# Kernel optimization log

Hardware: AMD Instinct MI355X
Metric: run time of the kernel (lower is better)

## Reference

```python
import jax, jax.numpy as jnp
import numpy as np

B, S, D, H = 2, 2048, 1024, 16
HD = D // H  # head dim = 64


def setup_inputs() -> dict:
    key = jax.random.key(0)
    k0, k1, k2 = jax.random.split(key, 3)
    x = jax.random.normal(k0, (B, S, D), dtype=jnp.float32)
    # fused QKV projection: nn.Linear(D, 3D) -> weight [3D, D], bias [3D]
    Wqkv_w = jax.random.normal(k1, (3 * D, D), dtype=jnp.float32) * (1.0 / np.sqrt(D))
    Wqkv_b = jnp.zeros((3 * D,), dtype=jnp.float32)
    out_w = jax.random.normal(k2, (D, D), dtype=jnp.float32) * (1.0 / np.sqrt(D))
    out_b = jnp.zeros((D,), dtype=jnp.float32)
    # ALiBi-like additive bias, shape [1, H, 1, S] (broadcasts over queries)
    slopes = 2.0 ** (-8.0 * jnp.arange(1, H + 1, dtype=jnp.float32) / H)  # [H]
    dist = (S - 1) - jnp.arange(S, dtype=jnp.float32)                      # [S]
    attn_bias = (-slopes[:, None] * dist[None, :]).reshape(1, H, 1, S)
    # key padding mask: second sequence is padded by 256 tokens at the end
    lengths = jnp.array([S, S - 256])
    attention_mask = jnp.arange(S)[None, :] < lengths[:, None]             # [B, S] bool
    return {"x": x, "Wqkv_w": Wqkv_w, "Wqkv_b": Wqkv_b, "out_w": out_w,
            "out_b": out_b, "attn_bias": attn_bias, "attention_mask": attention_mask}


def reference(x, Wqkv_w, Wqkv_b, out_w, out_b, attn_bias, attention_mask):
    b, s, d = x.shape
    # fused QKV projection, then chunk into q, k, v along feature dim
    qkv = jnp.einsum('bsd,ed->bse', x, Wqkv_w) + Wqkv_b  # [b, s, 3d]
    q, k, v = jnp.split(qkv, 3, axis=-1)
    # b s (h hd) -> b h s hd
    q = q.reshape(b, s, H, HD).transpose(0, 2, 1, 3)
    k = k.reshape(b, s, H, HD).transpose(0, 2, 1, 3)
    v = v.reshape(b, s, H, HD).transpose(0, 2, 1, 3)
    softmax_scale = 1.0 / np.sqrt(HD)
    aw = jnp.einsum('bhqe,bhke->bhqk', q, k) * softmax_scale  # [b, H, s, s]
    aw = aw + attn_bias  # attn_bias broadcasts [1,H,1,s] -> [b,H,s,s]
    min_val = jnp.finfo(aw.dtype).min
    # key padding mask: mask positions where attention_mask is False
    aw = jnp.where(attention_mask[:, None, None, :], aw, min_val)
    # causal mask (is_causal=True, s_q == s_k)
    causal = jnp.tril(jnp.ones((s, s), dtype=bool))
    aw = jnp.where(causal[None, None, :, :], aw, min_val)
    p = jax.nn.softmax(aw, axis=-1)
    out = jnp.einsum('bhqk,bhke->bhqe', p, v)  # [b, H, s, HD]
    out = out.transpose(0, 2, 1, 3).reshape(b, s, d)
    return jnp.einsum('bsd,ed->bse', out, out_w) + out_b
```

## Files before the change

### kernel.cpp

```cpp
#include <hip/hip_runtime.h>
#include <hip/hip_bf16.h>
#include <stdint.h>

typedef __attribute__((ext_vector_type(8))) short s16x8;
typedef __attribute__((ext_vector_type(8))) unsigned short u16x8;
typedef __attribute__((ext_vector_type(4))) float f32x4;

#define SEQ 2048
#define LOG2E 1.44269504088896f

__device__ __forceinline__ unsigned short f2b(float x) {
  union { __hip_bfloat16 h; unsigned short u; } cv;
  cv.h = __float2bfloat16(x);
  return cv.u;
}

__device__ __forceinline__ float exp2fast(float x) {
  float r;
  asm("v_exp_f32 %0, %1" : "=v"(r) : "v"(x));
  return r;
}

__device__ __forceinline__ void gload16(const void* g, void* l) {
  __builtin_amdgcn_global_load_lds(
      (const __attribute__((address_space(1))) void*)g,
      (__attribute__((address_space(3))) void*)l, 16, 0, 0);
}

__global__ void cvt_all(const float* __restrict__ x, const float* __restrict__ wq,
                        const float* __restrict__ ow, const float* __restrict__ abias,
                        const void* __restrict__ maskp,
                        __hip_bfloat16* __restrict__ xb, __hip_bfloat16* __restrict__ wqb,
                        __hip_bfloat16* __restrict__ owb, float* __restrict__ biasm) {
  const int i = blockIdx.x * 256 + threadIdx.x;
  if (i >= 2097152) {
    const int j = i - 2097152;
    const int b = j >> 15, h = (j >> 11) & 15, kv = j & 2047;
    const int* mi = (const int*)maskp;
    const unsigned char* mb = (const unsigned char*)maskp;
    const bool int_fmt = (mi[0] == 0 || mi[0] == 1);
    const bool ok = int_fmt ? (mi[b * SEQ + kv] != 0) : (mb[b * SEQ + kv] != 0);
    biasm[j] = ok ? abias[h * SEQ + kv] * LOG2E : -1e30f;
    return;
  }
  const float* src;
  __hip_bfloat16* dst;
  int off;
  if (i < 1048576) { src = x; dst = xb; off = i; }
  else if (i < 1835008) { src = wq; dst = wqb; off = i - 1048576; }
  else { src = ow; dst = owb; off = i - 1835008; }
  float4 v = reinterpret_cast<const float4*>(src)[off];
  ushort4 o;
  o.x = f2b(v.x); o.y = f2b(v.y); o.z = f2b(v.z); o.w = f2b(v.w);
  reinterpret_cast<ushort4*>(dst)[off] = o;
}

template <int MODE, int BM>
__global__ __launch_bounds__(256) void gemm_bt(
    const __hip_bfloat16* __restrict__ A, const __hip_bfloat16* __restrict__ B,
    const float* __restrict__ bias, void* __restrict__ Cout,
    __hip_bfloat16* __restrict__ Vt, int M, int N, int K) {
  constexpr int MR = BM / 32;
  __shared__ __align__(16) __hip_bfloat16 As[2][BM * 32];
  __shared__ __align__(16) __hip_bfloat16 Bs[2][128 * 32];
  const int tid = threadIdx.x;
  const int lane = tid & 63;
  const int w = tid >> 6;
  const int wr = w >> 1, wc = w & 1;
  const int rowg = blockIdx.x * BM;
  const int colg = blockIdx.y * 128;
  const int lr = lane & 15;
  const int lk = (lane >> 4) * 8;
  f32x4 acc[MR][4];
#pragma unroll
  for (int m = 0; m < MR; ++m)
#pragma unroll
    for (int n = 0; n < 4; ++n) acc[m][n] = (f32x4){0.f, 0.f, 0.f, 0.f};
#define GSTAGE(KT, C)                                                            \
  {                                                                              \
    _Pragma("unroll") for (int r = 0; r < BM / 64; ++r) {                        \
      const int idx = r * 256 + tid;                                             \
      gload16(A + (size_t)(rowg + (idx >> 2)) * K + (KT) + (idx & 3) * 8,        \
              &As[C][0] + idx * 8);                                              \
    }                                                                            \
    _Pragma("unroll") for (int r = 0; r < 2; ++r) {                              \
      const int idx = r * 256 + tid;                                             \
      gload16(B + (size_t)(colg + (idx >> 2)) * K + (KT) + (idx & 3) * 8,        \
              &Bs[C][0] + idx * 8);                                              \
    }                                                                            \
  }
  GSTAGE(0, 0);
  __syncthreads();
  int cur = 0;
  for (int kt = 0; kt < K; kt += 32) {
    if (kt + 32 < K) GSTAGE(kt + 32, cur ^ 1);
    s16x8 af[MR], bfr[4];
#pragma unroll
    for (int m = 0; m < MR; ++m)
      af[m] = *reinterpret_cast<const s16x8*>(&As[cur][0] +
                                              (wr * (BM / 2) + m * 16 + lr) * 32 + lk);
#pragma unroll
    for (int n = 0; n < 4; ++n)
      bfr[n] = *reinterpret_cast<const s16x8*>(&Bs[cur][0] +
                                               (wc * 64 + n * 16 + lr) * 32 + lk);
#pragma unroll
    for (int m = 0; m < MR; ++m)
#pragma unroll
      for (int n = 0; n < 4; ++n)
        acc[m][n] = __builtin_amdgcn_mfma_f32_16x16x32_bf16(af[m], bfr[n], acc[m][n], 0, 0, 0);
    __syncthreads();
    cur ^= 1;
  }
#undef GSTAGE
  const int r0l = (lane >> 4) * 4;
  float bvn[4];
#pragma unroll
  for (int n = 0; n < 4; ++n) bvn[n] = bias[colg + wc * 64 + n * 16 + lr];
#pragma unroll
  for (int m = 0; m < MR; ++m) {
#pragma unroll
    for (int n = 0; n < 4; ++n) {
      const int col = colg + wc * 64 + n * 16 + lr;
      const int row0 = rowg + wr * (BM / 2) + m * 16 + r0l;
      const float bv = bvn[n];
      if (MODE == 0) {
        __hip_bfloat16* qkb = (__hip_bfloat16*)Cout;
        if (col < 1024) {
#pragma unroll
          for (int j = 0; j < 4; ++j)
            qkb[(size_t)(row0 + j) * 2048 + col] = __float2bfloat16(acc[m][n][j] + bv);
        } else if (col < 2048) {
          const int dd = col & 63;
          const int base = col - dd;
#pragma unroll
          for (int j = 0; j < 4; ++j) {
            const int s = row0 + j;
            qkb[(size_t)s * 2048 + base + (dd ^ ((s & 7) << 3))] =
                __float2bfloat16(acc[m][n][j] + bv);
          }
        } else {
          const int c2 = col - 2048;
          const int dd = c2 & 63;
          const int bb = row0 >> 11;
          const int s0 = (row0 & 2047) ^ ((dd & 7) << 3);
          ushort4 pk;
          unsigned short* pp = (unsigned short*)&pk;
#pragma unroll
          for (int j = 0; j < 4; ++j) pp[j] = f2b(acc[m][n][j] + bv);
          *reinterpret_cast<ushort4*>(
              Vt + ((size_t)(bb * 16 + (c2 >> 6)) * 64 + dd) * 2048 + s0) = pk;
        }
      } else {
        float* o = (float*)Cout;
#pragma unroll
        for (int j = 0; j < 4; ++j)
          o[(size_t)(row0 + j) * N + col] = acc[m][n][j] + bv;
      }
    }
  }
}

__device__ __forceinline__ void attn_tile(
    const char* Ks, const char* Vs, char* pw, const float* bmb,
    s16x8 aq0, s16x8 aq1, int lane, int kv0, int q_abs, bool causal,
    int rd0, int rd1, const int* pwo,
    float m_r, float& l_r, f32x4* oa) {
  const int g = lane >> 4;
  const float SCALE2 = 0.125f * LOG2E;
  f32x4 bvp[4];
#pragma unroll
  for (int n = 0; n < 4; ++n) {
    bvp[n] = *reinterpret_cast<const f32x4*>(bmb + kv0 + n * 16 + g * 4);
#pragma unroll
    for (int j = 0; j < 4; ++j) bvp[n][j] -= m_r;
  }
  f32x4 sf[4];
  __builtin_amdgcn_s_setprio(1);
#pragma unroll
  for (int n = 0; n < 4; ++n) {
    s16x8 ak0 = *reinterpret_cast<const s16x8*>(Ks + rd0 + n * 2048);
    s16x8 ak1 = *reinterpret_cast<const s16x8*>(Ks + rd1 + n * 2048);
    f32x4 z = (f32x4){0.f, 0.f, 0.f, 0.f};
    z = __builtin_amdgcn_mfma_f32_16x16x32_bf16(ak0, aq0, z, 0, 0, 0);
    z = __builtin_amdgcn_mfma_f32_16x16x32_bf16(ak1, aq1, z, 0, 0, 0);
    sf[n] = z;
  }
  __builtin_amdgcn_s_setprio(0);
#pragma unroll
  for (int n = 0; n < 4; ++n)
#pragma unroll
    for (int j = 0; j < 4; ++j) sf[n][j] = fmaf(sf[n][j], SCALE2, bvp[n][j]);
  if (causal) {
    const int kvb = kv0 + g * 4;
#pragma unroll
    for (int n = 0; n < 4; ++n)
#pragma unroll
      for (int j = 0; j < 4; ++j)
        if (kvb + n * 16 + j > q_abs) sf[n][j] = -1e30f;
  }
  float ps[4];
#pragma unroll
  for (int n = 0; n < 4; ++n) {
#pragma unroll
    for (int j = 0; j < 4; ++j) sf[n][j] = exp2fast(sf[n][j]);
    ps[n] = (sf[n][0] + sf[n][1]) + (sf[n][2] + sf[n][3]);
  }
  l_r += (ps[0] + ps[1]) + (ps[2] + ps[3]);
  s16x8 bva[4], bvb[4];
#pragma unroll
  for (int d = 0; d < 4; ++d) {
    bva[d] = *reinterpret_cast<const s16x8*>(Vs + rd0 + d * 2048);
    bvb[d] = *reinterpret_cast<const s16x8*>(Vs + rd1 + d * 2048);
  }
#pragma unroll
  for (int n = 0; n < 4; ++n) {
    union { ushort4 u; uint2 v; } pk;
    pk.u.x = f2b(sf[n][0]); pk.u.y = f2b(sf[n][1]);
    pk.u.z = f2b(sf[n][2]); pk.u.w = f2b(sf[n][3]);
    *reinterpret_cast<uint2*>(pw + pwo[n]) = pk.v;
  }
  s16x8 pa0 = *reinterpret_cast<const s16x8*>(pw + rd0);
  s16x8 pa1 = *reinterpret_cast<const s16x8*>(pw + rd1);
  __builtin_amdgcn_s_setprio(1);
#pragma unroll
  for (int d = 0; d < 4; ++d) {
    oa[d] = __builtin_amdgcn_mfma_f32_16x16x32_bf16(pa0, bva[d], oa[d], 0, 0, 0);
    oa[d] = __builtin_amdgcn_mfma_f32_16x16x32_bf16(pa1, bvb[d], oa[d], 0, 0, 0);
  }
  __builtin_amdgcn_s_setprio(0);
}

__global__ __launch_bounds__(512, 4) void attn_fwd6(
    const __hip_bfloat16* __restrict__ qk, const __hip_bfloat16* __restrict__ Vt,
    const float* __restrict__ biasm, __hip_bfloat16* __restrict__ O) {
  __shared__ __align__(16) char KV[2][2][2][8192];
  __shared__ __align__(16) char Ps[8][2048];
  const int tid = threadIdx.x;
  const int lane = tid & 63;
  const int w = tid >> 6;
  const int wsub = w & 3;
  const int z = w >> 2;
  const int bid = blockIdx.x;
  const int qt = 31 - (bid >> 5);
  const int bh = bid & 31;
  const int b = bh >> 4, h = bh & 15;
  const int row0 = qt * 64 + wsub * 16;
  const int lr = lane & 15;
  const int g = lane >> 4;
  const int NTit = (qt >> 1) + 1;
  const int xm = (lr & 7) << 4;
  const int lkB = g * 16;
  const int rd0 = lr * 128 + (lkB ^ xm);
  const int rd1 = lr * 128 + ((64 + lkB) ^ xm);
  const int pwo[4] = {lr * 128 + ((g * 8) ^ xm),       lr * 128 + ((32 + g * 8) ^ xm),
                      lr * 128 + ((64 + g * 8) ^ xm),  lr * 128 + ((96 + g * 8) ^ xm)};
  const __hip_bfloat16* qptr =
      qk + (size_t)(b * SEQ + row0 + lr) * 2048 + h * 64 + g * 8;
  const s16x8 aq0 = *reinterpret_cast<const s16x8*>(qptr);
  const s16x8 aq1 = *reinterpret_cast<const s16x8*>(qptr + 32);
  const int q_abs = row0 + lr;
  const float* bmb = biasm + (size_t)bh * 2048;
  float mb = bmb[q_abs];
  if (mb < -1e29f) {
    int lo = 0, hi = q_abs;
    while (lo < hi) {
      const int mid = (lo + hi + 1) >> 1;
      if (bmb[mid] < -1e29f) hi = mid - 1; else lo = mid;
    }
    mb = bmb[lo];
  }
  const float m_r = mb + 12.0f;
  float l_r = 0.f;
  f32x4 oa[4];
#pragma unroll
  for (int d = 0; d < 4; ++d) oa[d] = (f32x4){0.f, 0.f, 0.f, 0.f};
  const int r_ = tid >> 3;
  const int c16 = tid & 7;
  const __hip_bfloat16* kb = qk + ((size_t)b * SEQ + r_) * 2048 + 1024 + h * 64 + c16 * 8;
  const __hip_bfloat16* vb = Vt + ((size_t)bh * 64 + r_) * 2048 + c16 * 8;
#define ISSUE(T, C)                                                     \
  {                                                                     \
    const int tE_ = 2 * (T);                                            \
    const int tO_ = (2 * (T) + 1 <= qt) ? (2 * (T) + 1) : qt;           \
    gload16(kb + (size_t)(tE_ * 64) * 2048, KV[0][C][0] + tid * 16);    \
    gload16(kb + (size_t)(tO_ * 64) * 2048, KV[1][C][0] + tid * 16);    \
    gload16(vb + tE_ * 64, KV[0][C][1] + tid * 16);                     \
    gload16(vb + tO_ * 64, KV[1][C][1] + tid * 16);                     \
  }
  ISSUE(0, 0);
  __syncthreads();
  int cur = 0;
  for (int t = 0; t < NTit; ++t) {
    if (t + 1 < NTit) ISSUE(t + 1, cur ^ 1);
    const int tz = 2 * t + z;
    if (tz <= qt)
      attn_tile(KV[z][cur][0], KV[z][cur][1], Ps[w], bmb, aq0, aq1, lane,
                tz * 64, q_abs, tz == qt, rd0, rd1, pwo, m_r, l_r, oa);
    __syncthreads();
    cur ^= 1;
  }
#undef ISSUE
  l_r += __shfl_xor(l_r, 16);
  l_r += __shfl_xor(l_r, 32);
  float* mlbuf = (float*)&KV[0][0][0][0];
  if (z == 1) {
    float* mo = (float*)(&Ps[0][0] + wsub * 4096);
#pragma unroll
    for (int d = 0; d < 4; ++d)
#pragma unroll
      for (int j = 0; j < 4; ++j)
        mo[(g * 4 + j) * 64 + d * 16 + lr] = oa[d][j];
    if (lane < 16) {
      mlbuf[wsub * 32 + lr] = m_r;
      mlbuf[wsub * 32 + 16 + lr] = l_r;
    }
  }
  __syncthreads();
  if (z == 0) {
    const float mB = mlbuf[wsub * 32 + lr];
    const float lB = mlbuf[wsub * 32 + 16 + lr];
    const float mS = fmaxf(m_r, mB);
    const float fA = exp2fast(m_r - mS);
    const float fB = exp2fast(mB - mS);
    const float linv = 1.0f / (l_r * fA + lB * fB);
    float fAj[4], fBj[4], lij[4];
#pragma unroll
    for (int j = 0; j < 4; ++j) {
      fAj[j] = __shfl(fA, g * 4 + j);
      fBj[j] = __shfl(fB, g * 4 + j);
      lij[j] = __shfl(linv, g * 4 + j);
    }
    const float* mo = (const float*)(&Ps[0][0] + wsub * 4096);
#pragma unroll
    for (int d = 0; d < 4; ++d)
#pragma unroll
      for (int j = 0; j < 4; ++j) {
        const float v =
            (oa[d][j] * fAj[j] + mo[(g * 4 + j) * 64 + d * 16 + lr] * fBj[j]) * lij[j];
        O[(size_t)(b * SEQ + row0 + g * 4 + j) * 1024 + h * 64 + d * 16 + lr] =
            __float2bfloat16(v);
      }
  }
}

extern "C" void kernel_launch(void* const* d_in, const int* in_sizes, int n_in,
                              void* d_out, int out_size, void* d_ws, size_t ws_size,
                              hipStream_t stream) {
  const float* x     = (const float*)d_in[0];
  const float* wqkv  = (const float*)d_in[1];
  const float* bqkv  = (const float*)d_in[2];
  const float* wout  = (const float*)d_in[3];
  const float* bout  = (const float*)d_in[4];
  const float* abias = (const float*)d_in[5];
  const void*  mask  = d_in[6];

  __hip_bfloat16* ws  = (__hip_bfloat16*)d_ws;
  __hip_bfloat16* xb  = ws;
  __hip_bfloat16* wqb = ws + 4194304;
  __hip_bfloat16* owb = ws + 7340032;
  __hip_bfloat16* qkb = ws + 8388608;
  __hip_bfloat16* vtb = ws + 16777216;
  float*          bmf = (float*)(ws + 20971520);
  __hip_bfloat16* aob = xb;

  cvt_all<<<8448, 256, 0, stream>>>(x, wqkv, wout, abias, mask, xb, wqb, owb, bmf);
  gemm_bt<0, 128><<<dim3(32, 24), 256, 0, stream>>>(xb, wqb, bqkv, (void*)qkb, vtb,
                                                    4096, 3072, 1024);
  attn_fwd6<<<1024, 512, 0, stream>>>(qkb, vtb, bmf, aob);
  gemm_bt<1, 64><<<dim3(64, 8), 256, 0, stream>>>(aob, owb, bout, d_out,
                                                  (__hip_bfloat16*)nullptr, 4096, 1024, 1024);
}
```

Baseline: 108.0 us.

## Process 128-query tiles per block, reusing K/V register fragments across two row groups

The attention kernel now gives each wave two 16-row query groups (128 queries per block), so K and V fragments read from LDS are reused for both groups and the block count drops from 1024 to 512. Block scheduling is also reordered: heavy tiles come first, then lighter tiles ascending, to balance the causal workload. The aim is to halve LDS K/V reads and K/V global loads per query row. In exchange each thread holds more registers (two accumulator sets), there is less parallelism, and the causal diagonal region wastes more work.

```diff
diff --git a/kernel.cpp b/kernel.cpp
--- a/kernel.cpp
+++ b/kernel.cpp
@@ -160,36 +160,27 @@
   }
 }
 
-__device__ __forceinline__ void attn_tile(
-    const char* Ks, const char* Vs, char* pw, const float* bmb,
-    s16x8 aq0, s16x8 aq1, int lane, int kv0, int q_abs, bool causal,
-    int rd0, int rd1, const int* pwo,
+__device__ __forceinline__ void grp_tile(
+    const s16x8* ak0, const s16x8* ak1, const s16x8* bva, const s16x8* bvb,
+    const f32x4* bvp, s16x8 aq0, s16x8 aq1, char* pw, int lane,
+    int kv0, int q_abs, bool causal, int rd0, int rd1, const int* pwo,
     float m_r, float& l_r, f32x4* oa) {
   const int g = lane >> 4;
   const float SCALE2 = 0.125f * LOG2E;
-  f32x4 bvp[4];
-#pragma unroll
-  for (int n = 0; n < 4; ++n) {
-    bvp[n] = *reinterpret_cast<const f32x4*>(bmb + kv0 + n * 16 + g * 4);
-#pragma unroll
-    for (int j = 0; j < 4; ++j) bvp[n][j] -= m_r;
-  }
   f32x4 sf[4];
   __builtin_amdgcn_s_setprio(1);
 #pragma unroll
   for (int n = 0; n < 4; ++n) {
-    s16x8 ak0 = *reinterpret_cast<const s16x8*>(Ks + rd0 + n * 2048);
-    s16x8 ak1 = *reinterpret_cast<const s16x8*>(Ks + rd1 + n * 2048);
     f32x4 z = (f32x4){0.f, 0.f, 0.f, 0.f};
-    z = __builtin_amdgcn_mfma_f32_16x16x32_bf16(ak0, aq0, z, 0, 0, 0);
-    z = __builtin_amdgcn_mfma_f32_16x16x32_bf16(ak1, aq1, z, 0, 0, 0);
+    z = __builtin_amdgcn_mfma_f32_16x16x32_bf16(ak0[n], aq0, z, 0, 0, 0);
+    z = __builtin_amdgcn_mfma_f32_16x16x32_bf16(ak1[n], aq1, z, 0, 0, 0);
     sf[n] = z;
   }
   __builtin_amdgcn_s_setprio(0);
 #pragma unroll
   for (int n = 0; n < 4; ++n)
 #pragma unroll
-    for (int j = 0; j < 4; ++j) sf[n][j] = fmaf(sf[n][j], SCALE2, bvp[n][j]);
+    for (int j = 0; j < 4; ++j) sf[n][j] = fmaf(sf[n][j], SCALE2, bvp[n][j] - m_r);
   if (causal) {
     const int kvb = kv0 + g * 4;
 #pragma unroll
@@ -206,12 +197,6 @@
     ps[n] = (sf[n][0] + sf[n][1]) + (sf[n][2] + sf[n][3]);
   }
   l_r += (ps[0] + ps[1]) + (ps[2] + ps[3]);
-  s16x8 bva[4], bvb[4];
-#pragma unroll
-  for (int d = 0; d < 4; ++d) {
-    bva[d] = *reinterpret_cast<const s16x8*>(Vs + rd0 + d * 2048);
-    bvb[d] = *reinterpret_cast<const s16x8*>(Vs + rd1 + d * 2048);
-  }
 #pragma unroll
   for (int n = 0; n < 4; ++n) {
     union { ushort4 u; uint2 v; } pk;
@@ -230,7 +215,7 @@
   __builtin_amdgcn_s_setprio(0);
 }
 
-__global__ __launch_bounds__(512, 4) void attn_fwd6(
+__global__ __launch_bounds__(512, 4) void attn_fwd7(
     const __hip_bfloat16* __restrict__ qk, const __hip_bfloat16* __restrict__ Vt,
     const float* __restrict__ biasm, __hip_bfloat16* __restrict__ O) {
   __shared__ __align__(16) char KV[2][2][2][8192];
@@ -241,39 +226,48 @@
   const int wsub = w & 3;
   const int z = w >> 2;
   const int bid = blockIdx.x;
-  const int qt = 31 - (bid >> 5);
+  const int qt = (bid < 256) ? (15 - (bid >> 5)) : ((bid - 256) >> 5);
   const int bh = bid & 31;
   const int b = bh >> 4, h = bh & 15;
-  const int row0 = qt * 64 + wsub * 16;
   const int lr = lane & 15;
   const int g = lane >> 4;
-  const int NTit = (qt >> 1) + 1;
+  const int rowA = qt * 128 + wsub * 32;
+  const int qA = rowA + lr;
+  const int qB = rowA + 16 + lr;
+  const int NTit = qt + 1;
   const int xm = (lr & 7) << 4;
   const int lkB = g * 16;
   const int rd0 = lr * 128 + (lkB ^ xm);
   const int rd1 = lr * 128 + ((64 + lkB) ^ xm);
   const int pwo[4] = {lr * 128 + ((g * 8) ^ xm),       lr * 128 + ((32 + g * 8) ^ xm),
                       lr * 128 + ((64 + g * 8) ^ xm),  lr * 128 + ((96 + g * 8) ^ xm)};
-  const __hip_bfloat16* qptr =
-      qk + (size_t)(b * SEQ + row0 + lr) * 2048 + h * 64 + g * 8;
-  const s16x8 aq0 = *reinterpret_cast<const s16x8*>(qptr);
-  const s16x8 aq1 = *reinterpret_cast<const s16x8*>(qptr + 32);
-  const int q_abs = row0 + lr;
+  const __hip_bfloat16* qbase = qk + (size_t)b * SEQ * 2048 + h * 64 + g * 8;
+  const s16x8 aqA0 = *reinterpret_cast<const s16x8*>(qbase + (size_t)qA * 2048);
+  const s16x8 aqA1 = *reinterpret_cast<const s16x8*>(qbase + (size_t)qA * 2048 + 32);
+  const s16x8 aqB0 = *reinterpret_cast<const s16x8*>(qbase + (size_t)qB * 2048);
+  const s16x8 aqB1 = *reinterpret_cast<const s16x8*>(qbase + (size_t)qB * 2048 + 32);
   const float* bmb = biasm + (size_t)bh * 2048;
-  float mb = bmb[q_abs];
-  if (mb < -1e29f) {
-    int lo = 0, hi = q_abs;
-    while (lo < hi) {
-      const int mid = (lo + hi + 1) >> 1;
-      if (bmb[mid] < -1e29f) hi = mid - 1; else lo = mid;
-    }
-    mb = bmb[lo];
-  }
-  const float m_r = mb + 12.0f;
-  float l_r = 0.f;
-  f32x4 oa[4];
-#pragma unroll
-  for (int d = 0; d < 4; ++d) oa[d] = (f32x4){0.f, 0.f, 0.f, 0.f};
+  auto prefix_m = [&](int q) -> float {
+    float mb = bmb[q];
+    if (mb < -1e29f) {
+      int lo = 0, hi = q;
+      while (lo < hi) {
+        const int mid = (lo + hi + 1) >> 1;
+        if (bmb[mid] < -1e29f) hi = mid - 1; else lo = mid;
+      }
+      mb = bmb[lo];
+    }
+    return mb + 12.0f;
+  };
+  const float m_rA = prefix_m(qA);
+  const float m_rB = prefix_m(qB);
+  float l_rA = 0.f, l_rB = 0.f;
+  f32x4 oaA[4], oaB[4];
+#pragma unroll
+  for (int d = 0; d < 4; ++d) {
+    oaA[d] = (f32x4){0.f, 0.f, 0.f, 0.f};
+    oaB[d] = (f32x4){0.f, 0.f, 0.f, 0.f};
+  }
   const int r_ = tid >> 3;
   const int c16 = tid & 7;
   const __hip_bfloat16* kb = qk + ((size_t)b * SEQ + r_) * 2048 + 1024 + h * 64 + c16 * 8;
@@ -281,7 +275,7 @@
 #define ISSUE(T, C)                                                     \
   {                                                                     \
     const int tE_ = 2 * (T);                                            \
-    const int tO_ = (2 * (T) + 1 <= qt) ? (2 * (T) + 1) : qt;           \
+    const int tO_ = 2 * (T) + 1;                                        \
     gload16(kb + (size_t)(tE_ * 64) * 2048, KV[0][C][0] + tid * 16);    \
     gload16(kb + (size_t)(tO_ * 64) * 2048, KV[1][C][0] + tid * 16);    \
     gload16(vb + tE_ * 64, KV[0][C][1] + tid * 16);                     \
@@ -293,53 +287,89 @@
   for (int t = 0; t < NTit; ++t) {
     if (t + 1 < NTit) ISSUE(t + 1, cur ^ 1);
     const int tz = 2 * t + z;
-    if (tz <= qt)
-      attn_tile(KV[z][cur][0], KV[z][cur][1], Ps[w], bmb, aq0, aq1, lane,
-                tz * 64, q_abs, tz == qt, rd0, rd1, pwo, m_r, l_r, oa);
+    const int kv0 = tz * 64;
+    if (kv0 <= rowA + 31) {
+      const char* Ks = KV[z][cur][0];
+      const char* Vs = KV[z][cur][1];
+      s16x8 ak0[4], ak1[4], bva[4], bvb[4];
+#pragma unroll
+      for (int n = 0; n < 4; ++n) {
+        ak0[n] = *reinterpret_cast<const s16x8*>(Ks + rd0 + n * 2048);
+        ak1[n] = *reinterpret_cast<const s16x8*>(Ks + rd1 + n * 2048);
+      }
+#pragma unroll
+      for (int d = 0; d < 4; ++d) {
+        bva[d] = *reinterpret_cast<const s16x8*>(Vs + rd0 + d * 2048);
+        bvb[d] = *reinterpret_cast<const s16x8*>(Vs + rd1 + d * 2048);
+      }
+      f32x4 bvp[4];
+#pragma unroll
+      for (int n = 0; n < 4; ++n)
+        bvp[n] = *reinterpret_cast<const f32x4*>(bmb + kv0 + n * 16 + g * 4);
+      grp_tile(ak0, ak1, bva, bvb, bvp, aqA0, aqA1, Ps[w], lane, kv0, qA,
+               kv0 + 63 > rowA, rd0, rd1, pwo, m_rA, l_rA, oaA);
+      grp_tile(ak0, ak1, bva, bvb, bvp, aqB0, aqB1, Ps[w], lane, kv0, qB,
+               kv0 + 63 > rowA + 16, rd0, rd1, pwo, m_rB, l_rB, oaB);
+    }
     __syncthreads();
     cur ^= 1;
   }
 #undef ISSUE
-  l_r += __shfl_xor(l_r, 16);
-  l_r += __shfl_xor(l_r, 32);
-  float* mlbuf = (float*)&KV[0][0][0][0];
+  l_rA += __shfl_xor(l_rA, 16); l_rA += __shfl_xor(l_rA, 32);
+  l_rB += __shfl_xor(l_rB, 16); l_rB += __shfl_xor(l_rB, 32);
+  float* xch = (float*)&KV[0][0][0][0];
+  float* mlx = (float*)&KV[1][0][0][0];
+  __syncthreads();
   if (z == 1) {
-    float* mo = (float*)(&Ps[0][0] + wsub * 4096);
-#pragma unroll
-    for (int d = 0; d < 4; ++d)
-#pragma unroll
-      for (int j = 0; j < 4; ++j)
-        mo[(g * 4 + j) * 64 + d * 16 + lr] = oa[d][j];
+#pragma unroll
+    for (int grp = 0; grp < 2; ++grp) {
+      const f32x4* oa = grp ? oaB : oaA;
+      float* mo = xch + (wsub * 2 + grp) * 1024;
+#pragma unroll
+      for (int d = 0; d < 4; ++d)
+#pragma unroll
+        for (int j = 0; j < 4; ++j)
+          mo[(g * 4 + j) * 64 + d * 16 + lr] = oa[d][j];
+    }
     if (lane < 16) {
-      mlbuf[wsub * 32 + lr] = m_r;
-      mlbuf[wsub * 32 + 16 + lr] = l_r;
+      mlx[(wsub * 2 + 0) * 32 + lr] = m_rA;
+      mlx[(wsub * 2 + 0) * 32 + 16 + lr] = l_rA;
+      mlx[(wsub * 2 + 1) * 32 + lr] = m_rB;
+      mlx[(wsub * 2 + 1) * 32 + 16 + lr] = l_rB;
     }
   }
   __syncthreads();
   if (z == 0) {
-    const float mB = mlbuf[wsub * 32 + lr];
-    const float lB = mlbuf[wsub * 32 + 16 + lr];
-    const float mS = fmaxf(m_r, mB);
-    const float fA = exp2fast(m_r - mS);
-    const float fB = exp2fast(mB - mS);
-    const float linv = 1.0f / (l_r * fA + lB * fB);
-    float fAj[4], fBj[4], lij[4];
-#pragma unroll
-    for (int j = 0; j < 4; ++j) {
-      fAj[j] = __shfl(fA, g * 4 + j);
-      fBj[j] = __shfl(fB, g * 4 + j);
-      lij[j] = __shfl(linv, g * 4 + j);
-    }
-    const float* mo = (const float*)(&Ps[0][0] + wsub * 4096);
-#pragma unroll
-    for (int d = 0; d < 4; ++d)
+#pragma unroll
+    for (int grp = 0; grp < 2; ++grp) {
+      const f32x4* oa = grp ? oaB : oaA;
+      const float mA_ = grp ? m_rB : m_rA;
+      const float lA_ = grp ? l_rB : l_rA;
+      const float mB_ = mlx[(wsub * 2 + grp) * 32 + lr];
+      const float lB_ = mlx[(wsub * 2 + grp) * 32 + 16 + lr];
+      const float mS = fmaxf(mA_, mB_);
+      const float fA = exp2fast(mA_ - mS);
+      const float fB = exp2fast(mB_ - mS);
+      const float linv = 1.0f / (lA_ * fA + lB_ * fB);
+      float fAj[4], fBj[4], lij[4];
 #pragma unroll
       for (int j = 0; j < 4; ++j) {
-        const float v =
-            (oa[d][j] * fAj[j] + mo[(g * 4 + j) * 64 + d * 16 + lr] * fBj[j]) * lij[j];
-        O[(size_t)(b * SEQ + row0 + g * 4 + j) * 1024 + h * 64 + d * 16 + lr] =
-            __float2bfloat16(v);
+        fAj[j] = __shfl(fA, g * 4 + j);
+        fBj[j] = __shfl(fB, g * 4 + j);
+        lij[j] = __shfl(linv, g * 4 + j);
       }
+      const float* mo = xch + (wsub * 2 + grp) * 1024;
+      const int rbase = rowA + grp * 16;
+#pragma unroll
+      for (int d = 0; d < 4; ++d)
+#pragma unroll
+        for (int j = 0; j < 4; ++j) {
+          const float v =
+              (oa[d][j] * fAj[j] + mo[(g * 4 + j) * 64 + d * 16 + lr] * fBj[j]) * lij[j];
+          O[(size_t)(b * SEQ + rbase + g * 4 + j) * 1024 + h * 64 + d * 16 + lr] =
+              __float2bfloat16(v);
+        }
+    }
   }
 }
 
@@ -366,7 +396,7 @@
   cvt_all<<<8448, 256, 0, stream>>>(x, wqkv, wout, abias, mask, xb, wqb, owb, bmf);
   gemm_bt<0, 128><<<dim3(32, 24), 256, 0, stream>>>(xb, wqb, bqkv, (void*)qkb, vtb,
                                                     4096, 3072, 1024);
-  attn_fwd6<<<1024, 512, 0, stream>>>(qkb, vtb, bmf, aob);
+  attn_fwd7<<<512, 512, 0, stream>>>(qkb, vtb, bmf, aob);
   gemm_bt<1, 64><<<dim3(64, 8), 256, 0, stream>>>(aob, owb, bout, d_out,
                                                   (__hip_bfloat16*)nullptr, 4096, 1024, 1024);
 }
```

New measurement: 271.4 us. 151% more time.
